# Kernel optimization log

Hardware: AMD Instinct MI355X
Metric: run time of the kernel (lower is better)

Reference implementation:

```python
import jax, jax.numpy as jnp
import numpy as np

E, TOP_K = 8, 2          # num_experts, num_experts_per_tok
B, S, H, I = 4, 2048, 1024, 4096  # batch, seq, hidden, intermediate
STD = 0.02


def setup_inputs() -> dict:
    key = jax.random.key(0)
    k0, k1, k2, k3 = jax.random.split(key, 4)
    return {
        "x": jax.random.normal(k0, (B, S, H), jnp.float32),
        "w_gate": jax.random.normal(k1, (E, H), jnp.float32) * STD,                 # gate: Linear(H->E, no bias)
        "w_fc": jax.random.normal(k2, (E, I, H), jnp.float32) * STD,                # c_fc per-expert [E, out, in]
        "b_fc": jnp.zeros((E, I), jnp.float32),
        "w_proj": jax.random.normal(k3, (E, H, I), jnp.float32) * (STD / np.sqrt(2 * 24)),  # c_proj, n_layer=24 init scale
        "b_proj": jnp.zeros((E, H), jnp.float32),
    }


def reference(x, w_gate, w_fc, b_fc, w_proj, b_proj):
    b, s, h = x.shape
    xf = x.reshape(-1, h)                       # [T, H], T = B*S
    T = xf.shape[0]

    # --- routing (softmax in fp32, top-k, renormalize) ---
    router_logits = xf @ w_gate.T               # [T, E]
    probs = jax.nn.softmax(router_logits.astype(jnp.float32), axis=-1)
    top_w, top_idx = jax.lax.top_k(probs, TOP_K)            # [T, K]
    top_w = top_w / jnp.sum(top_w, axis=-1, keepdims=True)  # normalize_expert_weights
    top_w = top_w.astype(x.dtype)

    # combine[t, e] = gate weight of expert e for token t (0 if not selected)
    combine = jnp.zeros((T, E), x.dtype).at[jnp.arange(T)[:, None], top_idx].add(top_w)

    # --- experts: weighted sum of per-expert MLPs (same math as sort/gather/scatter) ---
    out = jnp.zeros_like(xf)
    for e in range(E):
        ht = jax.nn.gelu(xf @ w_fc[e].T + b_fc[e], approximate=False)  # [T, I]
        ht = ht @ w_proj[e].T + b_proj[e]                              # [T, H]
        out = out + combine[:, e:e + 1] * ht

    return out.reshape(b, s, h), router_logits
```

## Files before the change

kernel.cpp:

```cpp
#include <hip/hip_runtime.h>
#include <hip/hip_bf16.h>
#include <math.h>

#define T_TOK 8192
#define HID 1024
#define IDIM 4096
#define NE 8
#define TK (T_TOK*2)

typedef __attribute__((ext_vector_type(8))) short short8;
typedef __attribute__((ext_vector_type(4))) float f32x4;

__device__ __forceinline__ void gld_lds16(const __hip_bfloat16* g, __hip_bfloat16* l)
{
    __builtin_amdgcn_global_load_lds(
        (const __attribute__((address_space(1))) void*)g,
        (__attribute__((address_space(3))) void*)l, 16, 0, 0);
}

__global__ __launch_bounds__(256) void cvt_kernel(const float* __restrict__ src,
                                                  __hip_bfloat16* __restrict__ dst, int n4)
{
    int i = blockIdx.x * 256 + threadIdx.x;
    int stride = gridDim.x * 256;
    for (; i < n4; i += stride) {
        float4 v = ((const float4*)src)[i];
        union { __hip_bfloat16 h[4]; ushort4 u; } t;
        t.h[0] = __float2bfloat16(v.x);
        t.h[1] = __float2bfloat16(v.y);
        t.h[2] = __float2bfloat16(v.z);
        t.h[3] = __float2bfloat16(v.w);
        ((ushort4*)dst)[i] = t.u;
    }
}

__global__ __launch_bounds__(64) void router_kernel(const float* __restrict__ x,
                                                    const float* __restrict__ wg,
                                                    float* __restrict__ logits_out,
                                                    int* __restrict__ top_idx,
                                                    float* __restrict__ top_w,
                                                    int* __restrict__ counts)
{
    int t = blockIdx.x;
    int lane = threadIdx.x;
    const float* xr = x + (size_t)t * HID;
    float acc[NE];
#pragma unroll
    for (int e = 0; e < NE; e++) acc[e] = 0.f;
    for (int h = lane; h < HID; h += 64) {
        float xv = xr[h];
#pragma unroll
        for (int e = 0; e < NE; e++) acc[e] += xv * wg[e * HID + h];
    }
#pragma unroll
    for (int e = 0; e < NE; e++)
        for (int off = 32; off > 0; off >>= 1)
            acc[e] += __shfl_down(acc[e], off, 64);
    if (lane == 0) {
        float mx = acc[0];
        for (int e = 1; e < NE; e++) mx = fmaxf(mx, acc[e]);
        float p[NE]; float s = 0.f;
        for (int e = 0; e < NE; e++) { p[e] = expf(acc[e] - mx); s += p[e]; }
        for (int e = 0; e < NE; e++) logits_out[(size_t)t * NE + e] = acc[e];
        int i1 = 0;
        for (int e = 1; e < NE; e++) if (p[e] > p[i1]) i1 = e;
        int i2 = -1;
        for (int e = 0; e < NE; e++) { if (e == i1) continue; if (i2 < 0 || p[e] > p[i2]) i2 = e; }
        float w1 = p[i1], w2 = p[i2], sw = w1 + w2;
        top_idx[t * 2] = i1; top_idx[t * 2 + 1] = i2;
        top_w[t * 2] = w1 / sw; top_w[t * 2 + 1] = w2 / sw;
        atomicAdd(&counts[i1], 1);
        atomicAdd(&counts[i2], 1);
    }
}

__global__ void scan_kernel(const int* __restrict__ counts, int* __restrict__ offsets)
{
    if (threadIdx.x == 0) {
        int s = 0;
        for (int e = 0; e < NE; e++) { offsets[e] = s; s += counts[e]; }
        offsets[NE] = s;
    }
}

__global__ __launch_bounds__(256) void scatter_kernel(const int* __restrict__ top_idx,
                                                      const float* __restrict__ top_w,
                                                      const int* __restrict__ offsets,
                                                      int* __restrict__ counts2,
                                                      int* __restrict__ expert_tok,
                                                      float* __restrict__ slot_w,
                                                      int* __restrict__ slot_of)
{
    int t = blockIdx.x * 256 + threadIdx.x;
    if (t >= T_TOK) return;
    for (int k = 0; k < 2; k++) {
        int e = top_idx[t * 2 + k];
        int pos = atomicAdd(&counts2[e], 1);
        int slot = offsets[e] + pos;
        expert_tok[slot] = t;
        slot_w[slot] = top_w[t * 2 + k];
        slot_of[t * 2 + k] = slot;
    }
}

__global__ __launch_bounds__(256) void gather_kernel(const float* __restrict__ x,
                                                     const int* __restrict__ expert_tok,
                                                     __hip_bfloat16* __restrict__ xg)
{
    int slot = blockIdx.x;
    int tok = expert_tok[slot];
    const float4* src = (const float4*)(x + (size_t)tok * HID);
    ushort4* dst = (ushort4*)(xg + (size_t)slot * HID);
    int h = threadIdx.x;
    float4 v = src[h];
    union { __hip_bfloat16 h4[4]; ushort4 u; } t;
    t.h4[0] = __float2bfloat16(v.x);
    t.h4[1] = __float2bfloat16(v.y);
    t.h4[2] = __float2bfloat16(v.z);
    t.h4[3] = __float2bfloat16(v.w);
    dst[h] = t.u;
}

template <int KDIM>
__device__ __forceinline__ void moe_gemm_loop(const __hip_bfloat16* __restrict__ A,
                                              int m0, int cnt,
                                              const __hip_bfloat16* __restrict__ B,
                                              __hip_bfloat16* Alds, __hip_bfloat16* Blds,
                                              f32x4 (&acc)[4][4])
{
    const int tid = threadIdx.x;
    const int lane = tid & 63, wave = tid >> 6;
    const int wm = (wave & 1) * 64, wn = (wave >> 1) * 64;
    const int fm = lane & 15, q = lane >> 4;

    const int srow = wave * 32 + (lane >> 2);
    const int schunk = (lane & 3) * 8;
    int ra0 = m0 + srow;      ra0 = (ra0 < cnt) ? ra0 : (cnt - 1);
    int ra1 = m0 + srow + 16; ra1 = (ra1 < cnt) ? ra1 : (cnt - 1);
    const __hip_bfloat16* gA0 = A + (size_t)ra0 * KDIM + schunk;
    const __hip_bfloat16* gA1 = A + (size_t)ra1 * KDIM + schunk;
    const __hip_bfloat16* gB0 = B + (size_t)srow * KDIM + schunk;
    const __hip_bfloat16* gB1 = B + (size_t)(srow + 16) * KDIM + schunk;
    __hip_bfloat16* lA0 = Alds + (wave * 32) * 32;
    __hip_bfloat16* lA1 = Alds + (wave * 32 + 16) * 32;
    __hip_bfloat16* lB0 = Blds + (wave * 32) * 32;
    __hip_bfloat16* lB1 = Blds + (wave * 32 + 16) * 32;

    for (int kt = 0; kt < KDIM / 32; ++kt) {
        __syncthreads();
        gld_lds16(gA0, lA0);
        gld_lds16(gA1, lA1);
        gld_lds16(gB0, lB0);
        gld_lds16(gB1, lB1);
        gA0 += 32; gA1 += 32; gB0 += 32; gB1 += 32;
        __syncthreads();

        short8 af[4], bfr[4];
#pragma unroll
        for (int mi = 0; mi < 4; mi++)
            af[mi] = *(const short8*)&Alds[(wm + mi * 16 + fm) * 32 + q * 8];
#pragma unroll
        for (int ni = 0; ni < 4; ni++)
            bfr[ni] = *(const short8*)&Blds[(wn + ni * 16 + fm) * 32 + q * 8];
#pragma unroll
        for (int mi = 0; mi < 4; mi++)
#pragma unroll
            for (int ni = 0; ni < 4; ni++)
                acc[mi][ni] = __builtin_amdgcn_mfma_f32_16x16x32_bf16(af[mi], bfr[ni],
                                                                      acc[mi][ni], 0, 0, 0);
    }
}

__global__ __launch_bounds__(256) void gemm_fc_kernel(const __hip_bfloat16* __restrict__ xg,
                                                      const __hip_bfloat16* __restrict__ wfc,
                                                      const float* __restrict__ b_fc,
                                                      const int* __restrict__ offsets,
                                                      __hip_bfloat16* __restrict__ ht)
{
    __shared__ __hip_bfloat16 Alds[128 * 32];
    __shared__ __hip_bfloat16 Blds[128 * 32];
    const int e = blockIdx.z;
    const int off = offsets[e];
    const int cnt = offsets[e + 1] - off;
    const int m0 = blockIdx.y * 128;
    if (m0 >= cnt) return;
    const int n0 = blockIdx.x * 128;

    f32x4 acc[4][4] = {};
    moe_gemm_loop<HID>(xg + (size_t)off * HID, m0, cnt,
                       wfc + (size_t)e * IDIM * HID + (size_t)n0 * HID, Alds, Blds, acc);

    const int tid = threadIdx.x, lane = tid & 63, wave = tid >> 6;
    const int wm = (wave & 1) * 64, wn = (wave >> 1) * 64, fm = lane & 15, q = lane >> 4;
#pragma unroll
    for (int ni = 0; ni < 4; ni++) {
        int n = n0 + wn + ni * 16 + fm;
        float bias = b_fc[(size_t)e * IDIM + n];
#pragma unroll
        for (int mi = 0; mi < 4; mi++) {
#pragma unroll
            for (int r = 0; r < 4; r++) {
                int m = m0 + wm + mi * 16 + q * 4 + r;
                if (m < cnt) {
                    float v = acc[mi][ni][r] + bias;
                    float g = 0.5f * v * (1.0f + erff(v * 0.70710678118654752f));
                    ht[(size_t)(off + m) * IDIM + n] = __float2bfloat16(g);
                }
            }
        }
    }
}

__global__ __launch_bounds__(256) void gemm_proj_kernel(const __hip_bfloat16* __restrict__ ht,
                                                        const __hip_bfloat16* __restrict__ wproj,
                                                        const float* __restrict__ b_proj,
                                                        const int* __restrict__ offsets,
                                                        const float* __restrict__ slot_w,
                                                        __hip_bfloat16* __restrict__ contrib)
{
    __shared__ __hip_bfloat16 Alds[128 * 32];
    __shared__ __hip_bfloat16 Blds[128 * 32];
    const int e = blockIdx.z;
    const int off = offsets[e];
    const int cnt = offsets[e + 1] - off;
    const int m0 = blockIdx.y * 128;
    if (m0 >= cnt) return;
    const int n0 = blockIdx.x * 128;

    f32x4 acc[4][4] = {};
    moe_gemm_loop<IDIM>(ht + (size_t)off * IDIM, m0, cnt,
                        wproj + (size_t)e * HID * IDIM + (size_t)n0 * IDIM, Alds, Blds, acc);

    const int tid = threadIdx.x, lane = tid & 63, wave = tid >> 6;
    const int wm = (wave & 1) * 64, wn = (wave >> 1) * 64, fm = lane & 15, q = lane >> 4;
#pragma unroll
    for (int mi = 0; mi < 4; mi++) {
#pragma unroll
        for (int r = 0; r < 4; r++) {
            int m = m0 + wm + mi * 16 + q * 4 + r;
            if (m >= cnt) continue;
            float sw = slot_w[off + m];
#pragma unroll
            for (int ni = 0; ni < 4; ni++) {
                int n = n0 + wn + ni * 16 + fm;
                float v = acc[mi][ni][r] + b_proj[(size_t)e * HID + n];
                contrib[(size_t)(off + m) * HID + n] = __float2bfloat16(v * sw);
            }
        }
    }
}

__global__ __launch_bounds__(256) void combine_kernel(const __hip_bfloat16* __restrict__ contrib,
                                                      const int* __restrict__ slot_of,
                                                      float* __restrict__ out)
{
    int t = blockIdx.x;
    int s0 = slot_of[t * 2], s1 = slot_of[t * 2 + 1];
    const ushort4* c0 = (const ushort4*)(contrib + (size_t)s0 * HID);
    const ushort4* c1 = (const ushort4*)(contrib + (size_t)s1 * HID);
    float4* o = (float4*)(out + (size_t)t * HID);
    int h = threadIdx.x;
    ushort4 a = c0[h], b = c1[h];
    union { unsigned u; float f; } f0, f1, f2, f3;
    f0.u = ((unsigned)a.x << 16); f1.u = ((unsigned)a.y << 16);
    f2.u = ((unsigned)a.z << 16); f3.u = ((unsigned)a.w << 16);
    union { unsigned u; float f; } g0, g1, g2, g3;
    g0.u = ((unsigned)b.x << 16); g1.u = ((unsigned)b.y << 16);
    g2.u = ((unsigned)b.z << 16); g3.u = ((unsigned)b.w << 16);
    float4 r;
    r.x = f0.f + g0.f; r.y = f1.f + g1.f; r.z = f2.f + g2.f; r.w = f3.f + g3.f;
    o[h] = r;
}

extern "C" void kernel_launch(void* const* d_in, const int* in_sizes, int n_in,
                              void* d_out, int out_size, void* d_ws, size_t ws_size,
                              hipStream_t stream)
{
    const float* x      = (const float*)d_in[0];
    const float* w_gate = (const float*)d_in[1];
    const float* w_fc   = (const float*)d_in[2];
    const float* b_fc   = (const float*)d_in[3];
    const float* w_proj = (const float*)d_in[4];
    const float* b_proj = (const float*)d_in[5];
    float* out = (float*)d_out;
    float* logits_out = out + (size_t)T_TOK * HID;

    char* ws = (char*)d_ws;
    const size_t WB = (size_t)NE * IDIM * HID * 2;
    size_t o_wfc     = 0;
    size_t o_wproj   = o_wfc + WB;
    size_t o_xg      = o_wproj + WB;
    size_t o_ht      = o_xg + (size_t)TK * HID * 2;
    size_t o_contrib = o_ht + (size_t)TK * IDIM * 2;
    size_t o_route   = o_contrib + (size_t)TK * HID * 2;

    __hip_bfloat16* wfc_b   = (__hip_bfloat16*)(ws + o_wfc);
    __hip_bfloat16* wproj_b = (__hip_bfloat16*)(ws + o_wproj);
    __hip_bfloat16* xg      = (__hip_bfloat16*)(ws + o_xg);
    __hip_bfloat16* ht      = (__hip_bfloat16*)(ws + o_ht);
    __hip_bfloat16* contrib = (__hip_bfloat16*)(ws + o_contrib);

    size_t ro = o_route;
    int*   top_idx    = (int*)(ws + ro);   ro += (size_t)T_TOK * 2 * 4;
    float* top_w      = (float*)(ws + ro); ro += (size_t)T_TOK * 2 * 4;
    int*   counts     = (int*)(ws + ro);   ro += NE * 4;
    int*   counts2    = (int*)(ws + ro);   ro += NE * 4;
    int*   offsets    = (int*)(ws + ro);   ro += 16 * 4;
    int*   expert_tok = (int*)(ws + ro);   ro += (size_t)TK * 4;
    float* slot_w     = (float*)(ws + ro); ro += (size_t)TK * 4;
    int*   slot_of    = (int*)(ws + ro);   ro += (size_t)T_TOK * 2 * 4;

    if (ws_size < ro) return;

    hipMemsetAsync(counts, 0, 2 * NE * sizeof(int), stream);

    const int n4 = NE * IDIM * HID / 4;
    cvt_kernel<<<2048, 256, 0, stream>>>(w_fc, wfc_b, n4);
    cvt_kernel<<<2048, 256, 0, stream>>>(w_proj, wproj_b, n4);

    router_kernel<<<T_TOK, 64, 0, stream>>>(x, w_gate, logits_out, top_idx, top_w, counts);
    scan_kernel<<<1, 64, 0, stream>>>(counts, offsets);
    scatter_kernel<<<T_TOK / 256, 256, 0, stream>>>(top_idx, top_w, offsets, counts2,
                                                    expert_tok, slot_w, slot_of);
    gather_kernel<<<TK, 256, 0, stream>>>(x, expert_tok, xg);

    gemm_fc_kernel<<<dim3(IDIM / 128, T_TOK / 128, NE), 256, 0, stream>>>(
        xg, wfc_b, b_fc, offsets, ht);
    gemm_proj_kernel<<<dim3(HID / 128, T_TOK / 128, NE), 256, 0, stream>>>(
        ht, wproj_b, b_proj, offsets, slot_w, contrib);

    combine_kernel<<<T_TOK, 256, 0, stream>>>(contrib, slot_of, out);
}
```

Baseline: 1.136 ms.

## Switch MoE expert GEMMs from bf16 to fp8 with fixed weight scales

Expert weights, gathered activations and the GELU intermediate are now quantized to fp8, with fixed scale factors on the weights. Both GEMMs use the fp8 16x16x32 MFMA with a 64-byte K tile, and the epilogues write vectorized rows using a transposed operand order. This halves weight and activation traffic and doubles MFMA throughput, at the cost of much lower precision that may break the accuracy tolerance. The router also packs four tokens per 256-thread block.

```diff
diff --git a/kernel.cpp b/kernel.cpp
--- a/kernel.cpp
+++ b/kernel.cpp
@@ -8,41 +8,42 @@
 #define NE 8
 #define TK (T_TOK*2)
 
-typedef __attribute__((ext_vector_type(8))) short short8;
+#define SF_FC   8.0f
+#define SF_PROJ 64.0f
+
 typedef __attribute__((ext_vector_type(4))) float f32x4;
 
-__device__ __forceinline__ void gld_lds16(const __hip_bfloat16* g, __hip_bfloat16* l)
+__device__ __forceinline__ void gld_lds16(const void* g, void* l)
 {
     __builtin_amdgcn_global_load_lds(
         (const __attribute__((address_space(1))) void*)g,
         (__attribute__((address_space(3))) void*)l, 16, 0, 0);
 }
 
-__global__ __launch_bounds__(256) void cvt_kernel(const float* __restrict__ src,
-                                                  __hip_bfloat16* __restrict__ dst, int n4)
+__global__ __launch_bounds__(256) void cvt8_kernel(const float* __restrict__ src,
+                                                   unsigned char* __restrict__ dst,
+                                                   int n4, float scale)
 {
     int i = blockIdx.x * 256 + threadIdx.x;
     int stride = gridDim.x * 256;
     for (; i < n4; i += stride) {
         float4 v = ((const float4*)src)[i];
-        union { __hip_bfloat16 h[4]; ushort4 u; } t;
-        t.h[0] = __float2bfloat16(v.x);
-        t.h[1] = __float2bfloat16(v.y);
-        t.h[2] = __float2bfloat16(v.z);
-        t.h[3] = __float2bfloat16(v.w);
-        ((ushort4*)dst)[i] = t.u;
-    }
-}
-
-__global__ __launch_bounds__(64) void router_kernel(const float* __restrict__ x,
-                                                    const float* __restrict__ wg,
-                                                    float* __restrict__ logits_out,
-                                                    int* __restrict__ top_idx,
-                                                    float* __restrict__ top_w,
-                                                    int* __restrict__ counts)
-{
-    int t = blockIdx.x;
-    int lane = threadIdx.x;
+        int d = 0;
+        d = __builtin_amdgcn_cvt_pk_fp8_f32(v.x * scale, v.y * scale, d, false);
+        d = __builtin_amdgcn_cvt_pk_fp8_f32(v.z * scale, v.w * scale, d, true);
+        ((int*)dst)[i] = d;
+    }
+}
+
+__global__ __launch_bounds__(256) void router_kernel(const float* __restrict__ x,
+                                                     const float* __restrict__ wg,
+                                                     float* __restrict__ logits_out,
+                                                     int* __restrict__ top_idx,
+                                                     float* __restrict__ top_w,
+                                                     int* __restrict__ counts)
+{
+    int wave = threadIdx.x >> 6, lane = threadIdx.x & 63;
+    int t = blockIdx.x * 4 + wave;
     const float* xr = x + (size_t)t * HID;
     float acc[NE];
 #pragma unroll
@@ -105,80 +106,78 @@
 
 __global__ __launch_bounds__(256) void gather_kernel(const float* __restrict__ x,
                                                      const int* __restrict__ expert_tok,
-                                                     __hip_bfloat16* __restrict__ xg)
+                                                     unsigned char* __restrict__ xg)
 {
     int slot = blockIdx.x;
     int tok = expert_tok[slot];
     const float4* src = (const float4*)(x + (size_t)tok * HID);
-    ushort4* dst = (ushort4*)(xg + (size_t)slot * HID);
+    int* dst = (int*)(xg + (size_t)slot * HID);
     int h = threadIdx.x;
     float4 v = src[h];
-    union { __hip_bfloat16 h4[4]; ushort4 u; } t;
-    t.h4[0] = __float2bfloat16(v.x);
-    t.h4[1] = __float2bfloat16(v.y);
-    t.h4[2] = __float2bfloat16(v.z);
-    t.h4[3] = __float2bfloat16(v.w);
-    dst[h] = t.u;
+    int d = 0;
+    d = __builtin_amdgcn_cvt_pk_fp8_f32(v.x, v.y, d, false);
+    d = __builtin_amdgcn_cvt_pk_fp8_f32(v.z, v.w, d, true);
+    dst[h] = d;
 }
 
 template <int KDIM>
-__device__ __forceinline__ void moe_gemm_loop(const __hip_bfloat16* __restrict__ A,
+__device__ __forceinline__ void moe_gemm_loop(const unsigned char* __restrict__ A,
                                               int m0, int cnt,
-                                              const __hip_bfloat16* __restrict__ B,
-                                              __hip_bfloat16* Alds, __hip_bfloat16* Blds,
+                                              const unsigned char* __restrict__ B,
+                                              unsigned char* Alds, unsigned char* Blds,
                                               f32x4 (&acc)[4][4])
 {
     const int tid = threadIdx.x;
     const int lane = tid & 63, wave = tid >> 6;
-    const int wm = (wave & 1) * 64, wn = (wave >> 1) * 64;
+    const int wt = (wave & 1) * 64, wn = (wave >> 1) * 64;
     const int fm = lane & 15, q = lane >> 4;
 
     const int srow = wave * 32 + (lane >> 2);
-    const int schunk = (lane & 3) * 8;
+    const int sbyte = (lane & 3) * 16;
     int ra0 = m0 + srow;      ra0 = (ra0 < cnt) ? ra0 : (cnt - 1);
     int ra1 = m0 + srow + 16; ra1 = (ra1 < cnt) ? ra1 : (cnt - 1);
-    const __hip_bfloat16* gA0 = A + (size_t)ra0 * KDIM + schunk;
-    const __hip_bfloat16* gA1 = A + (size_t)ra1 * KDIM + schunk;
-    const __hip_bfloat16* gB0 = B + (size_t)srow * KDIM + schunk;
-    const __hip_bfloat16* gB1 = B + (size_t)(srow + 16) * KDIM + schunk;
-    __hip_bfloat16* lA0 = Alds + (wave * 32) * 32;
-    __hip_bfloat16* lA1 = Alds + (wave * 32 + 16) * 32;
-    __hip_bfloat16* lB0 = Blds + (wave * 32) * 32;
-    __hip_bfloat16* lB1 = Blds + (wave * 32 + 16) * 32;
-
-    for (int kt = 0; kt < KDIM / 32; ++kt) {
+    const unsigned char* gA0 = A + (size_t)ra0 * KDIM + sbyte;
+    const unsigned char* gA1 = A + (size_t)ra1 * KDIM + sbyte;
+    const unsigned char* gB0 = B + (size_t)srow * KDIM + sbyte;
+    const unsigned char* gB1 = B + (size_t)(srow + 16) * KDIM + sbyte;
+    unsigned char* lA0 = Alds + (wave * 32) * 64;
+    unsigned char* lA1 = lA0 + 16 * 64;
+    unsigned char* lB0 = Blds + (wave * 32) * 64;
+    unsigned char* lB1 = lB0 + 16 * 64;
+
+    for (int kt = 0; kt < KDIM / 64; ++kt) {
         __syncthreads();
-        gld_lds16(gA0, lA0);
-        gld_lds16(gA1, lA1);
-        gld_lds16(gB0, lB0);
-        gld_lds16(gB1, lB1);
-        gA0 += 32; gA1 += 32; gB0 += 32; gB1 += 32;
+        gld_lds16(gA0, lA0); gld_lds16(gA1, lA1);
+        gld_lds16(gB0, lB0); gld_lds16(gB1, lB1);
+        gA0 += 64; gA1 += 64; gB0 += 64; gB1 += 64;
         __syncthreads();
-
-        short8 af[4], bfr[4];
-#pragma unroll
-        for (int mi = 0; mi < 4; mi++)
-            af[mi] = *(const short8*)&Alds[(wm + mi * 16 + fm) * 32 + q * 8];
-#pragma unroll
-        for (int ni = 0; ni < 4; ni++)
-            bfr[ni] = *(const short8*)&Blds[(wn + ni * 16 + fm) * 32 + q * 8];
-#pragma unroll
-        for (int mi = 0; mi < 4; mi++)
+#pragma unroll
+        for (int h = 0; h < 2; ++h) {
+            long wf[4], af[4];
 #pragma unroll
             for (int ni = 0; ni < 4; ni++)
-                acc[mi][ni] = __builtin_amdgcn_mfma_f32_16x16x32_bf16(af[mi], bfr[ni],
-                                                                      acc[mi][ni], 0, 0, 0);
-    }
-}
-
-__global__ __launch_bounds__(256) void gemm_fc_kernel(const __hip_bfloat16* __restrict__ xg,
-                                                      const __hip_bfloat16* __restrict__ wfc,
+                wf[ni] = *(const long*)&Blds[(wn + ni * 16 + fm) * 64 + h * 32 + q * 8];
+#pragma unroll
+            for (int mi = 0; mi < 4; mi++)
+                af[mi] = *(const long*)&Alds[(wt + mi * 16 + fm) * 64 + h * 32 + q * 8];
+#pragma unroll
+            for (int mi = 0; mi < 4; mi++)
+#pragma unroll
+                for (int ni = 0; ni < 4; ni++)
+                    acc[mi][ni] = __builtin_amdgcn_mfma_f32_16x16x32_fp8_fp8(
+                        wf[ni], af[mi], acc[mi][ni], 0, 0, 0);
+        }
+    }
+}
+
+__global__ __launch_bounds__(256) void gemm_fc_kernel(const unsigned char* __restrict__ xg,
+                                                      const unsigned char* __restrict__ wfc,
                                                       const float* __restrict__ b_fc,
                                                       const int* __restrict__ offsets,
-                                                      __hip_bfloat16* __restrict__ ht)
-{
-    __shared__ __hip_bfloat16 Alds[128 * 32];
-    __shared__ __hip_bfloat16 Blds[128 * 32];
+                                                      unsigned char* __restrict__ ht)
+{
+    __shared__ unsigned char Alds[128 * 64];
+    __shared__ unsigned char Blds[128 * 64];
     const int e = blockIdx.z;
     const int off = offsets[e];
     const int cnt = offsets[e + 1] - off;
@@ -191,35 +190,40 @@
                        wfc + (size_t)e * IDIM * HID + (size_t)n0 * HID, Alds, Blds, acc);
 
     const int tid = threadIdx.x, lane = tid & 63, wave = tid >> 6;
-    const int wm = (wave & 1) * 64, wn = (wave >> 1) * 64, fm = lane & 15, q = lane >> 4;
-#pragma unroll
-    for (int ni = 0; ni < 4; ni++) {
-        int n = n0 + wn + ni * 16 + fm;
-        float bias = b_fc[(size_t)e * IDIM + n];
-#pragma unroll
-        for (int mi = 0; mi < 4; mi++) {
+    const int wt = (wave & 1) * 64, wn = (wave >> 1) * 64, fm = lane & 15, q = lane >> 4;
+    const float inv = 1.0f / SF_FC;
+#pragma unroll
+    for (int mi = 0; mi < 4; mi++) {
+        int m = m0 + wt + mi * 16 + fm;
+        if (m >= cnt) continue;
+        unsigned char* row = ht + (size_t)(off + m) * IDIM + n0 + wn;
+#pragma unroll
+        for (int ni = 0; ni < 4; ni++) {
+            int nb = ni * 16 + q * 4;
+            float4 bias = *(const float4*)&b_fc[(size_t)e * IDIM + n0 + wn + nb];
+            float g[4];
 #pragma unroll
             for (int r = 0; r < 4; r++) {
-                int m = m0 + wm + mi * 16 + q * 4 + r;
-                if (m < cnt) {
-                    float v = acc[mi][ni][r] + bias;
-                    float g = 0.5f * v * (1.0f + erff(v * 0.70710678118654752f));
-                    ht[(size_t)(off + m) * IDIM + n] = __float2bfloat16(g);
-                }
+                float v = acc[mi][ni][r] * inv + ((const float*)&bias)[r];
+                g[r] = 0.5f * v * (1.0f + erff(v * 0.70710678118654752f));
             }
+            int d = 0;
+            d = __builtin_amdgcn_cvt_pk_fp8_f32(g[0], g[1], d, false);
+            d = __builtin_amdgcn_cvt_pk_fp8_f32(g[2], g[3], d, true);
+            *(int*)&row[nb] = d;
         }
     }
 }
 
-__global__ __launch_bounds__(256) void gemm_proj_kernel(const __hip_bfloat16* __restrict__ ht,
-                                                        const __hip_bfloat16* __restrict__ wproj,
+__global__ __launch_bounds__(256) void gemm_proj_kernel(const unsigned char* __restrict__ ht,
+                                                        const unsigned char* __restrict__ wproj,
                                                         const float* __restrict__ b_proj,
                                                         const int* __restrict__ offsets,
                                                         const float* __restrict__ slot_w,
                                                         __hip_bfloat16* __restrict__ contrib)
 {
-    __shared__ __hip_bfloat16 Alds[128 * 32];
-    __shared__ __hip_bfloat16 Blds[128 * 32];
+    __shared__ unsigned char Alds[128 * 64];
+    __shared__ unsigned char Blds[128 * 64];
     const int e = blockIdx.z;
     const int off = offsets[e];
     const int cnt = offsets[e + 1] - off;
@@ -232,20 +236,25 @@
                         wproj + (size_t)e * HID * IDIM + (size_t)n0 * IDIM, Alds, Blds, acc);
 
     const int tid = threadIdx.x, lane = tid & 63, wave = tid >> 6;
-    const int wm = (wave & 1) * 64, wn = (wave >> 1) * 64, fm = lane & 15, q = lane >> 4;
+    const int wt = (wave & 1) * 64, wn = (wave >> 1) * 64, fm = lane & 15, q = lane >> 4;
+    const float inv = 1.0f / SF_PROJ;
 #pragma unroll
     for (int mi = 0; mi < 4; mi++) {
-#pragma unroll
-        for (int r = 0; r < 4; r++) {
-            int m = m0 + wm + mi * 16 + q * 4 + r;
-            if (m >= cnt) continue;
-            float sw = slot_w[off + m];
-#pragma unroll
-            for (int ni = 0; ni < 4; ni++) {
-                int n = n0 + wn + ni * 16 + fm;
-                float v = acc[mi][ni][r] + b_proj[(size_t)e * HID + n];
-                contrib[(size_t)(off + m) * HID + n] = __float2bfloat16(v * sw);
+        int m = m0 + wt + mi * 16 + fm;
+        if (m >= cnt) continue;
+        float sw = slot_w[off + m];
+        __hip_bfloat16* row = contrib + (size_t)(off + m) * HID + n0 + wn;
+#pragma unroll
+        for (int ni = 0; ni < 4; ni++) {
+            int nb = ni * 16 + q * 4;
+            float4 bias = *(const float4*)&b_proj[(size_t)e * HID + n0 + wn + nb];
+            union { __hip_bfloat16 h[4]; ushort4 u; } t;
+#pragma unroll
+            for (int r = 0; r < 4; r++) {
+                float v = (acc[mi][ni][r] * inv + ((const float*)&bias)[r]) * sw;
+                t.h[r] = __float2bfloat16(v);
             }
+            *(ushort4*)&row[nb] = t.u;
         }
     }
 }
@@ -261,10 +270,9 @@
     float4* o = (float4*)(out + (size_t)t * HID);
     int h = threadIdx.x;
     ushort4 a = c0[h], b = c1[h];
-    union { unsigned u; float f; } f0, f1, f2, f3;
+    union { unsigned u; float f; } f0, f1, f2, f3, g0, g1, g2, g3;
     f0.u = ((unsigned)a.x << 16); f1.u = ((unsigned)a.y << 16);
     f2.u = ((unsigned)a.z << 16); f3.u = ((unsigned)a.w << 16);
-    union { unsigned u; float f; } g0, g1, g2, g3;
     g0.u = ((unsigned)b.x << 16); g1.u = ((unsigned)b.y << 16);
     g2.u = ((unsigned)b.z << 16); g3.u = ((unsigned)b.w << 16);
     float4 r;
@@ -286,18 +294,18 @@
     float* logits_out = out + (size_t)T_TOK * HID;
 
     char* ws = (char*)d_ws;
-    const size_t WB = (size_t)NE * IDIM * HID * 2;
+    const size_t WB8 = (size_t)NE * IDIM * HID;
     size_t o_wfc     = 0;
-    size_t o_wproj   = o_wfc + WB;
-    size_t o_xg      = o_wproj + WB;
-    size_t o_ht      = o_xg + (size_t)TK * HID * 2;
-    size_t o_contrib = o_ht + (size_t)TK * IDIM * 2;
+    size_t o_wproj   = o_wfc + WB8;
+    size_t o_xg      = o_wproj + WB8;
+    size_t o_ht      = o_xg + (size_t)TK * HID;
+    size_t o_contrib = o_ht + (size_t)TK * IDIM;
     size_t o_route   = o_contrib + (size_t)TK * HID * 2;
 
-    __hip_bfloat16* wfc_b   = (__hip_bfloat16*)(ws + o_wfc);
-    __hip_bfloat16* wproj_b = (__hip_bfloat16*)(ws + o_wproj);
-    __hip_bfloat16* xg      = (__hip_bfloat16*)(ws + o_xg);
-    __hip_bfloat16* ht      = (__hip_bfloat16*)(ws + o_ht);
+    unsigned char* wfc8   = (unsigned char*)(ws + o_wfc);
+    unsigned char* wproj8 = (unsigned char*)(ws + o_wproj);
+    unsigned char* xg     = (unsigned char*)(ws + o_xg);
+    unsigned char* ht     = (unsigned char*)(ws + o_ht);
     __hip_bfloat16* contrib = (__hip_bfloat16*)(ws + o_contrib);
 
     size_t ro = o_route;
@@ -315,19 +323,19 @@
     hipMemsetAsync(counts, 0, 2 * NE * sizeof(int), stream);
 
     const int n4 = NE * IDIM * HID / 4;
-    cvt_kernel<<<2048, 256, 0, stream>>>(w_fc, wfc_b, n4);
-    cvt_kernel<<<2048, 256, 0, stream>>>(w_proj, wproj_b, n4);
-
-    router_kernel<<<T_TOK, 64, 0, stream>>>(x, w_gate, logits_out, top_idx, top_w, counts);
+    cvt8_kernel<<<2048, 256, 0, stream>>>(w_fc, wfc8, n4, SF_FC);
+    cvt8_kernel<<<2048, 256, 0, stream>>>(w_proj, wproj8, n4, SF_PROJ);
+
+    router_kernel<<<T_TOK / 4, 256, 0, stream>>>(x, w_gate, logits_out, top_idx, top_w, counts);
     scan_kernel<<<1, 64, 0, stream>>>(counts, offsets);
     scatter_kernel<<<T_TOK / 256, 256, 0, stream>>>(top_idx, top_w, offsets, counts2,
                                                     expert_tok, slot_w, slot_of);
     gather_kernel<<<TK, 256, 0, stream>>>(x, expert_tok, xg);
 
     gemm_fc_kernel<<<dim3(IDIM / 128, T_TOK / 128, NE), 256, 0, stream>>>(
-        xg, wfc_b, b_fc, offsets, ht);
+        xg, wfc8, b_fc, offsets, ht);
     gemm_proj_kernel<<<dim3(HID / 128, T_TOK / 128, NE), 256, 0, stream>>>(
-        ht, wproj_b, b_proj, offsets, slot_w, contrib);
+        ht, wproj8, b_proj, offsets, slot_w, contrib);
 
     combine_kernel<<<T_TOK, 256, 0, stream>>>(contrib, slot_of, out);
 }
```

Result: slower. 1.306 ms (+15.0%).

## Swizzle LDS tiles, transpose MFMA operands for vector stores, remap proj grid

Applied to the files above, without the earlier changes.

The shared GEMM loop XOR-swizzles the 16-byte chunk placement in LDS so fragment reads avoid bank conflicts. It also swaps the MFMA operand order so each lane holds four consecutive output columns, which lets both epilogues issue packed 4-wide bf16 stores and float4 bias loads instead of scalar writes. The proj GEMM now uses a flattened 1D grid with a remapped block order so blocks that share a weight tile run close together for L2 reuse. The router packs four tokens per 256-thread block. The risk is a mismatch between the global-to-LDS swizzle and the read swizzle, which would silently corrupt results.

```diff
diff --git a/kernel.cpp b/kernel.cpp
--- a/kernel.cpp
+++ b/kernel.cpp
@@ -11,7 +11,7 @@
 typedef __attribute__((ext_vector_type(8))) short short8;
 typedef __attribute__((ext_vector_type(4))) float f32x4;
 
-__device__ __forceinline__ void gld_lds16(const __hip_bfloat16* g, __hip_bfloat16* l)
+__device__ __forceinline__ void gld_lds16(const void* g, void* l)
 {
     __builtin_amdgcn_global_load_lds(
         (const __attribute__((address_space(1))) void*)g,
@@ -34,15 +34,15 @@
     }
 }
 
-__global__ __launch_bounds__(64) void router_kernel(const float* __restrict__ x,
-                                                    const float* __restrict__ wg,
-                                                    float* __restrict__ logits_out,
-                                                    int* __restrict__ top_idx,
-                                                    float* __restrict__ top_w,
-                                                    int* __restrict__ counts)
-{
-    int t = blockIdx.x;
-    int lane = threadIdx.x;
+__global__ __launch_bounds__(256) void router_kernel(const float* __restrict__ x,
+                                                     const float* __restrict__ wg,
+                                                     float* __restrict__ logits_out,
+                                                     int* __restrict__ top_idx,
+                                                     float* __restrict__ top_w,
+                                                     int* __restrict__ counts)
+{
+    int wave = threadIdx.x >> 6, lane = threadIdx.x & 63;
+    int t = blockIdx.x * 4 + wave;
     const float* xr = x + (size_t)t * HID;
     float acc[NE];
 #pragma unroll
@@ -130,44 +130,43 @@
 {
     const int tid = threadIdx.x;
     const int lane = tid & 63, wave = tid >> 6;
-    const int wm = (wave & 1) * 64, wn = (wave >> 1) * 64;
+    const int wt = (wave & 1) * 64, wn = (wave >> 1) * 64;
     const int fm = lane & 15, q = lane >> 4;
+    const int csw = (q ^ ((fm >> 1) & 3)) * 8;
 
     const int srow = wave * 32 + (lane >> 2);
-    const int schunk = (lane & 3) * 8;
+    const int cg = ((lane & 3) ^ ((lane >> 3) & 3)) * 8;
     int ra0 = m0 + srow;      ra0 = (ra0 < cnt) ? ra0 : (cnt - 1);
     int ra1 = m0 + srow + 16; ra1 = (ra1 < cnt) ? ra1 : (cnt - 1);
-    const __hip_bfloat16* gA0 = A + (size_t)ra0 * KDIM + schunk;
-    const __hip_bfloat16* gA1 = A + (size_t)ra1 * KDIM + schunk;
-    const __hip_bfloat16* gB0 = B + (size_t)srow * KDIM + schunk;
-    const __hip_bfloat16* gB1 = B + (size_t)(srow + 16) * KDIM + schunk;
+    const __hip_bfloat16* gA0 = A + (size_t)ra0 * KDIM + cg;
+    const __hip_bfloat16* gA1 = A + (size_t)ra1 * KDIM + cg;
+    const __hip_bfloat16* gB0 = B + (size_t)srow * KDIM + cg;
+    const __hip_bfloat16* gB1 = B + (size_t)(srow + 16) * KDIM + cg;
     __hip_bfloat16* lA0 = Alds + (wave * 32) * 32;
-    __hip_bfloat16* lA1 = Alds + (wave * 32 + 16) * 32;
+    __hip_bfloat16* lA1 = lA0 + 16 * 32;
     __hip_bfloat16* lB0 = Blds + (wave * 32) * 32;
-    __hip_bfloat16* lB1 = Blds + (wave * 32 + 16) * 32;
+    __hip_bfloat16* lB1 = lB0 + 16 * 32;
 
     for (int kt = 0; kt < KDIM / 32; ++kt) {
         __syncthreads();
-        gld_lds16(gA0, lA0);
-        gld_lds16(gA1, lA1);
-        gld_lds16(gB0, lB0);
-        gld_lds16(gB1, lB1);
+        gld_lds16(gA0, lA0); gld_lds16(gA1, lA1);
+        gld_lds16(gB0, lB0); gld_lds16(gB1, lB1);
         gA0 += 32; gA1 += 32; gB0 += 32; gB1 += 32;
         __syncthreads();
 
-        short8 af[4], bfr[4];
+        short8 tf[4], wf[4];
 #pragma unroll
         for (int mi = 0; mi < 4; mi++)
-            af[mi] = *(const short8*)&Alds[(wm + mi * 16 + fm) * 32 + q * 8];
+            tf[mi] = *(const short8*)&Alds[(wt + mi * 16 + fm) * 32 + csw];
 #pragma unroll
         for (int ni = 0; ni < 4; ni++)
-            bfr[ni] = *(const short8*)&Blds[(wn + ni * 16 + fm) * 32 + q * 8];
+            wf[ni] = *(const short8*)&Blds[(wn + ni * 16 + fm) * 32 + csw];
 #pragma unroll
         for (int mi = 0; mi < 4; mi++)
 #pragma unroll
             for (int ni = 0; ni < 4; ni++)
-                acc[mi][ni] = __builtin_amdgcn_mfma_f32_16x16x32_bf16(af[mi], bfr[ni],
-                                                                      acc[mi][ni], 0, 0, 0);
+                acc[mi][ni] = __builtin_amdgcn_mfma_f32_16x16x32_bf16(
+                    wf[ni], tf[mi], acc[mi][ni], 0, 0, 0);
     }
 }
 
@@ -191,22 +190,23 @@
                        wfc + (size_t)e * IDIM * HID + (size_t)n0 * HID, Alds, Blds, acc);
 
     const int tid = threadIdx.x, lane = tid & 63, wave = tid >> 6;
-    const int wm = (wave & 1) * 64, wn = (wave >> 1) * 64, fm = lane & 15, q = lane >> 4;
-#pragma unroll
-    for (int ni = 0; ni < 4; ni++) {
-        int n = n0 + wn + ni * 16 + fm;
-        float bias = b_fc[(size_t)e * IDIM + n];
-#pragma unroll
-        for (int mi = 0; mi < 4; mi++) {
+    const int wt = (wave & 1) * 64, wn = (wave >> 1) * 64, fm = lane & 15, q = lane >> 4;
+#pragma unroll
+    for (int mi = 0; mi < 4; mi++) {
+        int m = m0 + wt + mi * 16 + fm;
+        if (m >= cnt) continue;
+        __hip_bfloat16* row = ht + (size_t)(off + m) * IDIM + n0 + wn;
+#pragma unroll
+        for (int ni = 0; ni < 4; ni++) {
+            int nb = ni * 16 + q * 4;
+            float4 bias = *(const float4*)&b_fc[(size_t)e * IDIM + n0 + wn + nb];
+            union { __hip_bfloat16 h[4]; ushort4 u; } t;
 #pragma unroll
             for (int r = 0; r < 4; r++) {
-                int m = m0 + wm + mi * 16 + q * 4 + r;
-                if (m < cnt) {
-                    float v = acc[mi][ni][r] + bias;
-                    float g = 0.5f * v * (1.0f + erff(v * 0.70710678118654752f));
-                    ht[(size_t)(off + m) * IDIM + n] = __float2bfloat16(g);
-                }
+                float v = acc[mi][ni][r] + ((const float*)&bias)[r];
+                t.h[r] = __float2bfloat16(0.5f * v * (1.0f + erff(v * 0.70710678118654752f)));
             }
+            *(ushort4*)&row[nb] = t.u;
         }
     }
 }
@@ -220,32 +220,39 @@
 {
     __shared__ __hip_bfloat16 Alds[128 * 32];
     __shared__ __hip_bfloat16 Blds[128 * 32];
-    const int e = blockIdx.z;
+    const int f = blockIdx.x;
+    const int x = f & 7, j = (f >> 3) & 7, H = f >> 6;
+    const int G = H * 8 + x;
+    const int e = G >> 6, mb = G & 63, nbk = j;
     const int off = offsets[e];
     const int cnt = offsets[e + 1] - off;
-    const int m0 = blockIdx.y * 128;
+    const int m0 = mb * 128;
     if (m0 >= cnt) return;
-    const int n0 = blockIdx.x * 128;
+    const int n0 = nbk * 128;
 
     f32x4 acc[4][4] = {};
     moe_gemm_loop<IDIM>(ht + (size_t)off * IDIM, m0, cnt,
                         wproj + (size_t)e * HID * IDIM + (size_t)n0 * IDIM, Alds, Blds, acc);
 
     const int tid = threadIdx.x, lane = tid & 63, wave = tid >> 6;
-    const int wm = (wave & 1) * 64, wn = (wave >> 1) * 64, fm = lane & 15, q = lane >> 4;
+    const int wt = (wave & 1) * 64, wn = (wave >> 1) * 64, fm = lane & 15, q = lane >> 4;
 #pragma unroll
     for (int mi = 0; mi < 4; mi++) {
-#pragma unroll
-        for (int r = 0; r < 4; r++) {
-            int m = m0 + wm + mi * 16 + q * 4 + r;
-            if (m >= cnt) continue;
-            float sw = slot_w[off + m];
-#pragma unroll
-            for (int ni = 0; ni < 4; ni++) {
-                int n = n0 + wn + ni * 16 + fm;
-                float v = acc[mi][ni][r] + b_proj[(size_t)e * HID + n];
-                contrib[(size_t)(off + m) * HID + n] = __float2bfloat16(v * sw);
+        int m = m0 + wt + mi * 16 + fm;
+        if (m >= cnt) continue;
+        float sw = slot_w[off + m];
+        __hip_bfloat16* row = contrib + (size_t)(off + m) * HID + n0 + wn;
+#pragma unroll
+        for (int ni = 0; ni < 4; ni++) {
+            int nb = ni * 16 + q * 4;
+            float4 bias = *(const float4*)&b_proj[(size_t)e * HID + n0 + wn + nb];
+            union { __hip_bfloat16 h[4]; ushort4 u; } t;
+#pragma unroll
+            for (int r = 0; r < 4; r++) {
+                float v = (acc[mi][ni][r] + ((const float*)&bias)[r]) * sw;
+                t.h[r] = __float2bfloat16(v);
             }
+            *(ushort4*)&row[nb] = t.u;
         }
     }
 }
@@ -261,10 +268,9 @@
     float4* o = (float4*)(out + (size_t)t * HID);
     int h = threadIdx.x;
     ushort4 a = c0[h], b = c1[h];
-    union { unsigned u; float f; } f0, f1, f2, f3;
+    union { unsigned u; float f; } f0, f1, f2, f3, g0, g1, g2, g3;
     f0.u = ((unsigned)a.x << 16); f1.u = ((unsigned)a.y << 16);
     f2.u = ((unsigned)a.z << 16); f3.u = ((unsigned)a.w << 16);
-    union { unsigned u; float f; } g0, g1, g2, g3;
     g0.u = ((unsigned)b.x << 16); g1.u = ((unsigned)b.y << 16);
     g2.u = ((unsigned)b.z << 16); g3.u = ((unsigned)b.w << 16);
     float4 r;
@@ -318,7 +324,7 @@
     cvt_kernel<<<2048, 256, 0, stream>>>(w_fc, wfc_b, n4);
     cvt_kernel<<<2048, 256, 0, stream>>>(w_proj, wproj_b, n4);
 
-    router_kernel<<<T_TOK, 64, 0, stream>>>(x, w_gate, logits_out, top_idx, top_w, counts);
+    router_kernel<<<T_TOK / 4, 256, 0, stream>>>(x, w_gate, logits_out, top_idx, top_w, counts);
     scan_kernel<<<1, 64, 0, stream>>>(counts, offsets);
     scatter_kernel<<<T_TOK / 256, 256, 0, stream>>>(top_idx, top_w, offsets, counts2,
                                                     expert_tok, slot_w, slot_of);
@@ -326,7 +332,7 @@
 
     gemm_fc_kernel<<<dim3(IDIM / 128, T_TOK / 128, NE), 256, 0, stream>>>(
         xg, wfc_b, b_fc, offsets, ht);
-    gemm_proj_kernel<<<dim3(HID / 128, T_TOK / 128, NE), 256, 0, stream>>>(
+    gemm_proj_kernel<<<NE * 64 * 8, 256, 0, stream>>>(
         ht, wproj_b, b_proj, offsets, slot_w, contrib);
 
     combine_kernel<<<T_TOK, 256, 0, stream>>>(contrib, slot_of, out);
```

After: 1.068 ms. 1.06x faster.
